# Optimization experiments

Hardware: AMD Instinct MI355X
Metric: run time of the kernel (lower is better)

The kernel has to match this reference:

```python
import jax, jax.numpy as jnp
import numpy as np

N, K = 50000, 16
D_IN, D_EDGE, D_HID, D_OUT = 128, 64, 32, 128


def setup_inputs() -> dict:
    key = jax.random.key(0)
    ks = jax.random.split(key, 10)
    s = lambda fan_in: 1.0 / np.sqrt(fan_in)
    return {
        'x': jax.random.normal(ks[0], (N, D_IN), jnp.float32),
        'neibs': jax.random.normal(ks[1], (N * K, D_IN), jnp.float32),
        'edge_emb': jax.random.normal(ks[2], (N * K, D_EDGE), jnp.float32),
        'mask': (jax.random.uniform(ks[3], (N, K)) < 0.3).astype(jnp.float32),
        # att: Linear(D_IN->H) -> tanh -> Linear(H->H); stored as [in,out]
        'W_att1_a': jax.random.uniform(ks[4], (D_IN, D_HID), jnp.float32, -s(D_IN), s(D_IN)),
        'W_att1_b': jax.random.uniform(ks[5], (D_HID, D_HID), jnp.float32, -s(D_HID), s(D_HID)),
        # att2 operates on concat(neibs, edge_emb)
        'W_att2_a': jax.random.uniform(ks[6], (D_IN + D_EDGE, D_HID), jnp.float32, -s(D_IN + D_EDGE), s(D_IN + D_EDGE)),
        'W_att2_b': jax.random.uniform(ks[7], (D_HID, D_HID), jnp.float32, -s(D_HID), s(D_HID)),
        'W_fc_x': jax.random.uniform(ks[8], (D_IN, D_OUT), jnp.float32, -s(D_IN), s(D_IN)),
        'W_fc_neib': jax.random.uniform(ks[9], (D_IN + D_EDGE, D_OUT), jnp.float32, -s(D_IN + D_EDGE), s(D_IN + D_EDGE)),
    }


def reference(x, neibs, edge_emb, mask, W_att1_a, W_att1_b, W_att2_a, W_att2_b, W_fc_x, W_fc_neib):
    n, k = mask.shape
    ne = jnp.concatenate([neibs, edge_emb], axis=1)            # [N*K, D_IN+D_EDGE]
    neib_att = jnp.tanh(ne @ W_att2_a) @ W_att2_b               # [N*K, H]
    x_att = jnp.tanh(x @ W_att1_a) @ W_att1_b                   # [N, H]
    ws = jnp.einsum('nkh,nh->nk', neib_att.reshape(n, k, -1), x_att)
    ws = jax.nn.softmax(ws + (-9999999.0) * mask, axis=1)       # masked softmax over neighbors
    agg_neib = jnp.einsum('nkd,nk->nd', ne.reshape(n, k, -1), ws)
    out = jnp.concatenate([x @ W_fc_x, agg_neib @ W_fc_neib], axis=1)  # concat_node=True
    return jax.nn.elu(out)  # dropout p=0.0 (eval), batchnorm=False
```

## Files before the change

### kernel.cpp

```cpp
#include <hip/hip_runtime.h>
#include <math.h>


typedef _Float16 half_t;
typedef __attribute__((ext_vector_type(4))) _Float16 half4_t;
typedef __attribute__((ext_vector_type(8))) _Float16 half8_t;
typedef __attribute__((ext_vector_type(4))) float f32x4;

#define NN   50000
#define GK   16
#define DIN  128
#define DED  64
#define DNE  192
#define G    8
#define NEP  200

#define WS_M    0
#define WS_W1A  4096
#define WS_W2A  12288
#define WS_WFX  24576
#define WS_WFN  57344

__device__ __forceinline__ void swz(const float* __restrict__ W, int ncol, int S,
                                    half_t* __restrict__ dst, int tid, int nth) {
  int T = ncol >> 4;
  int total = T * S * 512;
  for (int i = tid; i < total; i += nth) {
    int j = i & 7;
    int l = (i >> 3) & 63;
    int rest = i >> 9;
    int s = rest % S;
    int t = rest / S;
    int k = 32 * s + (l >> 4) * 8 + j;
    int n = 16 * t + (l & 15);
    dst[i] = (half_t)W[k * ncol + n];
  }
}

__global__ void setup_kernel(const float* __restrict__ W1a, const float* __restrict__ W1b,
                             const float* __restrict__ W2a, const float* __restrict__ W2b,
                             const float* __restrict__ Wfx, const float* __restrict__ Wfn,
                             unsigned char* __restrict__ ws) {
  int tid = blockIdx.x * blockDim.x + threadIdx.x;
  int nth = gridDim.x * blockDim.x;
  float* Mm = (float*)(ws + WS_M);
  for (int i = tid; i < 1024; i += nth) {
    int a = i >> 5, h = i & 31;
    float acc = 0.f;
    for (int h2 = 0; h2 < 32; ++h2)
      acc = fmaf(W1b[a * 32 + h2], W2b[h * 32 + h2], acc);
    Mm[i] = acc;
  }
  swz(W1a, 32, 4, (half_t*)(ws + WS_W1A), tid, nth);
  swz(W2a, 32, 6, (half_t*)(ws + WS_W2A), tid, nth);
  swz(Wfx, 128, 4, (half_t*)(ws + WS_WFX), tid, nth);
  swz(Wfn, 128, 6, (half_t*)(ws + WS_WFN), tid, nth);
}

__device__ __forceinline__ half8_t cvt8(float4 a, float4 b) {
  half8_t r;
  r[0] = (half_t)a.x; r[1] = (half_t)a.y; r[2] = (half_t)a.z; r[3] = (half_t)a.w;
  r[4] = (half_t)b.x; r[5] = (half_t)b.y; r[6] = (half_t)b.z; r[7] = (half_t)b.w;
  return r;
}

__device__ __forceinline__ float elu(float v) { return v > 0.f ? v : expm1f(v); }

__global__ __launch_bounds__(512, 4)
void attn_kernel(const float* __restrict__ x, const float* __restrict__ neibs,
                 const float* __restrict__ edge, const float* __restrict__ mask,
                 const unsigned char* __restrict__ ws, float* __restrict__ out) {
  __shared__ half_t neL[G * GK * NEP];
  __shared__ half_t aggL[16 * NEP];
  __shared__ float t1L[G][33];
  __shared__ float uL[G][33];
  __shared__ float scL[G][16];
  __shared__ float wsmL[G][16];

  const int tid = threadIdx.x;
  const int wave = tid >> 6;
  const int lane = tid & 63;
  const int l15 = lane & 15;
  const int q = lane >> 4;
  const int n0 = blockIdx.x * G;

  const float* Mm = (const float*)(ws + WS_M);
  const half_t* w1a = (const half_t*)(ws + WS_W1A);
  const half_t* w2a = (const half_t*)(ws + WS_W2A);
  const half_t* wfx = (const half_t*)(ws + WS_WFX);
  const half_t* wfn = (const half_t*)(ws + WS_WFN);

  {
    const float4* gn = (const float4*)(neibs + (size_t)n0 * (GK * DIN));
#pragma unroll
    for (int c = 0; c < 8; ++c) {
      int v = c * 512 + tid;
      float4 f = gn[v];
      int g = v >> 9, rem = v & 511, k = rem >> 5, d4 = rem & 31;
      half4_t h = { (half_t)f.x, (half_t)f.y, (half_t)f.z, (half_t)f.w };
      *(half4_t*)&neL[(g * GK + k) * NEP + d4 * 4] = h;
    }
    const float4* ge = (const float4*)(edge + (size_t)n0 * (GK * DED));
#pragma unroll
    for (int c = 0; c < 4; ++c) {
      int v = c * 512 + tid;
      float4 f = ge[v];
      int g = v >> 8, rem = v & 255, k = rem >> 4, d4 = rem & 15;
      half4_t h = { (half_t)f.x, (half_t)f.y, (half_t)f.z, (half_t)f.w };
      *(half4_t*)&neL[(g * GK + k) * NEP + DIN + d4 * 4] = h;
    }
    for (int i = tid; i < 16 * NEP / 2; i += 512)
      ((unsigned int*)aggL)[i] = 0u;
  }

  if (wave < 2) {
    f32x4 acc = {0.f, 0.f, 0.f, 0.f};
    int row = n0 + l15; if (row >= NN) row = NN - 1;
    const float* xrow = x + (size_t)row * DIN;
#pragma unroll
    for (int s = 0; s < 4; ++s) {
      float4 a0 = *(const float4*)(xrow + 32 * s + 8 * q);
      float4 a1 = *(const float4*)(xrow + 32 * s + 8 * q + 4);
      half8_t A = cvt8(a0, a1);
      half8_t B = *(const half8_t*)(w1a + ((size_t)(wave * 4 + s) * 64 + lane) * 8);
      acc = __builtin_amdgcn_mfma_f32_16x16x32_f16(A, B, acc, 0, 0, 0);
    }
#pragma unroll
    for (int r = 0; r < 4; ++r) {
      int g = 4 * q + r;
      if (g < G) t1L[g][wave * 16 + l15] = tanhf(acc[r]);
    }
  }
  __syncthreads();

  if (tid < G * 32) {
    int g = tid >> 5, h = tid & 31;
    float acc = 0.f;
#pragma unroll
    for (int a = 0; a < 32; ++a)
      acc = fmaf(t1L[g][a], Mm[a * 32 + h], acc);
    uL[g][h] = acc;
  }
  __syncthreads();

  {
    const int g = wave;
    f32x4 acc0 = {0.f, 0.f, 0.f, 0.f}, acc1 = {0.f, 0.f, 0.f, 0.f};
    const half_t* nerow = &neL[(g * GK + l15) * NEP];
#pragma unroll
    for (int s = 0; s < 6; ++s) {
      half8_t A  = *(const half8_t*)(nerow + 32 * s + 8 * q);
      half8_t B0 = *(const half8_t*)(w2a + ((size_t)(0 * 6 + s) * 64 + lane) * 8);
      half8_t B1 = *(const half8_t*)(w2a + ((size_t)(1 * 6 + s) * 64 + lane) * 8);
      acc0 = __builtin_amdgcn_mfma_f32_16x16x32_f16(A, B0, acc0, 0, 0, 0);
      acc1 = __builtin_amdgcn_mfma_f32_16x16x32_f16(A, B1, acc1, 0, 0, 0);
    }
    float u0 = uL[g][l15], u1 = uL[g][16 + l15];
    float sv[4];
#pragma unroll
    for (int r = 0; r < 4; ++r)
      sv[r] = tanhf(acc0[r]) * u0 + tanhf(acc1[r]) * u1;
#pragma unroll
    for (int off = 1; off <= 8; off <<= 1)
#pragma unroll
      for (int r = 0; r < 4; ++r)
        sv[r] += __shfl_xor(sv[r], off);
    if (l15 == 0)
#pragma unroll
      for (int r = 0; r < 4; ++r)
        scL[g][4 * q + r] = sv[r];
  }
  __syncthreads();

  {
    const int g = wave;
    float sc = -3.4e38f;
    if (lane < 16)
      sc = scL[g][lane] - 9999999.0f * mask[(size_t)(n0 + g) * GK + lane];
    float mx = sc;
#pragma unroll
    for (int off = 1; off <= 8; off <<= 1) mx = fmaxf(mx, __shfl_xor(mx, off));
    float e = (lane < 16) ? expf(sc - mx) : 0.f;
    float sm = e;
#pragma unroll
    for (int off = 1; off <= 8; off <<= 1) sm += __shfl_xor(sm, off);
    if (lane < 16) wsmL[g][lane] = e / sm;

    float a0 = 0.f, a1 = 0.f, a2 = 0.f;
    for (int k = 0; k < GK; ++k) {
      float wv = wsmL[g][k];
      const half_t* r_ = &neL[(g * GK + k) * NEP];
      a0 = fmaf(wv, (float)r_[lane], a0);
      a1 = fmaf(wv, (float)r_[64 + lane], a1);
      a2 = fmaf(wv, (float)r_[128 + lane], a2);
    }
    aggL[g * NEP + lane] = (half_t)a0;
    aggL[g * NEP + 64 + lane] = (half_t)a1;
    aggL[g * NEP + 128 + lane] = (half_t)a2;
  }
  __syncthreads();

  {
    f32x4 accx = {0.f, 0.f, 0.f, 0.f}, accn = {0.f, 0.f, 0.f, 0.f};
    int row = n0 + l15; if (row >= NN) row = NN - 1;
    const float* xrow = x + (size_t)row * DIN;
#pragma unroll
    for (int s = 0; s < 4; ++s) {
      float4 a0 = *(const float4*)(xrow + 32 * s + 8 * q);
      float4 a1 = *(const float4*)(xrow + 32 * s + 8 * q + 4);
      half8_t A = cvt8(a0, a1);
      half8_t B = *(const half8_t*)(wfx + ((size_t)(wave * 4 + s) * 64 + lane) * 8);
      accx = __builtin_amdgcn_mfma_f32_16x16x32_f16(A, B, accx, 0, 0, 0);
    }
#pragma unroll
    for (int s = 0; s < 6; ++s) {
      half8_t A = *(const half8_t*)(&aggL[l15 * NEP + 32 * s + 8 * q]);
      half8_t B = *(const half8_t*)(wfn + ((size_t)(wave * 6 + s) * 64 + lane) * 8);
      accn = __builtin_amdgcn_mfma_f32_16x16x32_f16(A, B, accn, 0, 0, 0);
    }
#pragma unroll
    for (int r = 0; r < 4; ++r) {
      int m = 4 * q + r;
      if (m < G) {
        size_t base = (size_t)(n0 + m) * 256;
        out[base + wave * 16 + l15] = elu(accx[r]);
        out[base + 128 + wave * 16 + l15] = elu(accn[r]);
      }
    }
  }
}

extern "C" void kernel_launch(void* const* d_in, const int* in_sizes, int n_in,
                              void* d_out, int out_size, void* d_ws, size_t ws_size,
                              hipStream_t stream) {
  const float* x     = (const float*)d_in[0];
  const float* neibs = (const float*)d_in[1];
  const float* edge  = (const float*)d_in[2];
  const float* mask  = (const float*)d_in[3];
  const float* W1a   = (const float*)d_in[4];
  const float* W1b   = (const float*)d_in[5];
  const float* W2a   = (const float*)d_in[6];
  const float* W2b   = (const float*)d_in[7];
  const float* Wfx   = (const float*)d_in[8];
  const float* Wfn   = (const float*)d_in[9];
  float* out = (float*)d_out;
  unsigned char* ws = (unsigned char*)d_ws;

  hipLaunchKernelGGL(setup_kernel, dim3(64), dim3(256), 0, stream,
                     W1a, W1b, W2a, W2b, Wfx, Wfn, ws);
  hipLaunchKernelGGL(attn_kernel, dim3(NN / G), dim3(512), 0, stream,
                     x, neibs, edge, mask, ws, out);
}
```

Measured before the change: 764.8 us.

## Split x-projection into pre-kernel and drop LDS staging of neighbor features

A new pre_kernel computes the x @ W_fc_x half of the output and the per-node attention query vector u. It stashes u temporarily in the not-yet-written second half of the output buffer. The attention kernel now assigns one node per wave and feeds neighbor and edge rows directly from global memory into the MFMA. It then re-reads them from global (expected to hit cache) for the softmax-weighted aggregation, instead of staging everything as fp16 in a large shared buffer. This cuts shared memory use sharply to raise occupancy, at the cost of a second pass over neighbor data and an extra kernel launch.

```diff
diff --git a/kernel.cpp b/kernel.cpp
--- a/kernel.cpp
+++ b/kernel.cpp
@@ -12,8 +12,6 @@
 #define DIN  128
 #define DED  64
 #define DNE  192
-#define G    8
-#define NEP  200
 
 #define WS_M    0
 #define WS_W1A  4096
@@ -66,167 +64,166 @@
 
 __device__ __forceinline__ float elu(float v) { return v > 0.f ? v : expm1f(v); }
 
-__global__ __launch_bounds__(512, 4)
-void attn_kernel(const float* __restrict__ x, const float* __restrict__ neibs,
-                 const float* __restrict__ edge, const float* __restrict__ mask,
-                 const unsigned char* __restrict__ ws, float* __restrict__ out) {
-  __shared__ half_t neL[G * GK * NEP];
-  __shared__ half_t aggL[16 * NEP];
-  __shared__ float t1L[G][33];
-  __shared__ float uL[G][33];
-  __shared__ float scL[G][16];
-  __shared__ float wsmL[G][16];
-
+__global__ __launch_bounds__(256, 4)
+void pre_kernel(const float* __restrict__ x, const unsigned char* __restrict__ ws,
+                float* __restrict__ out) {
+  __shared__ float t1L[64][33];
   const int tid = threadIdx.x;
-  const int wave = tid >> 6;
-  const int lane = tid & 63;
-  const int l15 = lane & 15;
-  const int q = lane >> 4;
-  const int n0 = blockIdx.x * G;
-
+  const int wave = tid >> 6, lane = tid & 63;
+  const int l15 = lane & 15, q = lane >> 4;
+  const int nb0 = blockIdx.x * 64;
+  const int n0 = nb0 + wave * 16;
   const float* Mm = (const float*)(ws + WS_M);
   const half_t* w1a = (const half_t*)(ws + WS_W1A);
-  const half_t* w2a = (const half_t*)(ws + WS_W2A);
   const half_t* wfx = (const half_t*)(ws + WS_WFX);
-  const half_t* wfn = (const half_t*)(ws + WS_WFN);
-
-  {
-    const float4* gn = (const float4*)(neibs + (size_t)n0 * (GK * DIN));
-#pragma unroll
-    for (int c = 0; c < 8; ++c) {
-      int v = c * 512 + tid;
-      float4 f = gn[v];
-      int g = v >> 9, rem = v & 511, k = rem >> 5, d4 = rem & 31;
-      half4_t h = { (half_t)f.x, (half_t)f.y, (half_t)f.z, (half_t)f.w };
-      *(half4_t*)&neL[(g * GK + k) * NEP + d4 * 4] = h;
-    }
-    const float4* ge = (const float4*)(edge + (size_t)n0 * (GK * DED));
-#pragma unroll
-    for (int c = 0; c < 4; ++c) {
-      int v = c * 512 + tid;
-      float4 f = ge[v];
-      int g = v >> 8, rem = v & 255, k = rem >> 4, d4 = rem & 15;
-      half4_t h = { (half_t)f.x, (half_t)f.y, (half_t)f.z, (half_t)f.w };
-      *(half4_t*)&neL[(g * GK + k) * NEP + DIN + d4 * 4] = h;
-    }
-    for (int i = tid; i < 16 * NEP / 2; i += 512)
-      ((unsigned int*)aggL)[i] = 0u;
-  }
-
-  if (wave < 2) {
-    f32x4 acc = {0.f, 0.f, 0.f, 0.f};
-    int row = n0 + l15; if (row >= NN) row = NN - 1;
-    const float* xrow = x + (size_t)row * DIN;
-#pragma unroll
-    for (int s = 0; s < 4; ++s) {
-      float4 a0 = *(const float4*)(xrow + 32 * s + 8 * q);
-      float4 a1 = *(const float4*)(xrow + 32 * s + 8 * q + 4);
-      half8_t A = cvt8(a0, a1);
-      half8_t B = *(const half8_t*)(w1a + ((size_t)(wave * 4 + s) * 64 + lane) * 8);
-      acc = __builtin_amdgcn_mfma_f32_16x16x32_f16(A, B, acc, 0, 0, 0);
-    }
-#pragma unroll
-    for (int r = 0; r < 4; ++r) {
-      int g = 4 * q + r;
-      if (g < G) t1L[g][wave * 16 + l15] = tanhf(acc[r]);
-    }
+
+  int row = n0 + l15; if (row >= NN) row = NN - 1;
+  const float* xrow = x + (size_t)row * DIN;
+  half8_t Ax[4];
+  f32x4 t0acc = {0.f, 0.f, 0.f, 0.f}, t1acc = {0.f, 0.f, 0.f, 0.f};
+#pragma unroll
+  for (int s = 0; s < 4; ++s) {
+    float4 a0 = *(const float4*)(xrow + 32 * s + 8 * q);
+    float4 a1 = *(const float4*)(xrow + 32 * s + 8 * q + 4);
+    Ax[s] = cvt8(a0, a1);
+    half8_t B0 = *(const half8_t*)(w1a + ((size_t)(0 * 4 + s) * 64 + lane) * 8);
+    half8_t B1 = *(const half8_t*)(w1a + ((size_t)(1 * 4 + s) * 64 + lane) * 8);
+    t0acc = __builtin_amdgcn_mfma_f32_16x16x32_f16(Ax[s], B0, t0acc, 0, 0, 0);
+    t1acc = __builtin_amdgcn_mfma_f32_16x16x32_f16(Ax[s], B1, t1acc, 0, 0, 0);
+  }
+#pragma unroll
+  for (int r = 0; r < 4; ++r) {
+    t1L[wave * 16 + 4 * q + r][l15]      = tanhf(t0acc[r]);
+    t1L[wave * 16 + 4 * q + r][16 + l15] = tanhf(t1acc[r]);
   }
   __syncthreads();
 
-  if (tid < G * 32) {
-    int g = tid >> 5, h = tid & 31;
+#pragma unroll
+  for (int i = 0; i < 8; ++i) {
+    int idx = i * 256 + tid;
+    int g = idx >> 5, h = idx & 31;
     float acc = 0.f;
 #pragma unroll
     for (int a = 0; a < 32; ++a)
       acc = fmaf(t1L[g][a], Mm[a * 32 + h], acc);
-    uL[g][h] = acc;
-  }
+    int n = nb0 + g;
+    if (n < NN) out[(size_t)n * 256 + 128 + h] = acc;
+  }
+
+#pragma unroll
+  for (int t = 0; t < 8; ++t) {
+    f32x4 acc = {0.f, 0.f, 0.f, 0.f};
+#pragma unroll
+    for (int s = 0; s < 4; ++s) {
+      half8_t B = *(const half8_t*)(wfx + ((size_t)(t * 4 + s) * 64 + lane) * 8);
+      acc = __builtin_amdgcn_mfma_f32_16x16x32_f16(Ax[s], B, acc, 0, 0, 0);
+    }
+#pragma unroll
+    for (int r = 0; r < 4; ++r) {
+      int m = n0 + 4 * q + r;
+      if (m < NN) out[(size_t)m * 256 + t * 16 + l15] = elu(acc[r]);
+    }
+  }
+}
+
+__global__ __launch_bounds__(512, 6)
+void attn_kernel(const float* __restrict__ neibs, const float* __restrict__ edge,
+                 const float* __restrict__ mask, const unsigned char* __restrict__ ws,
+                 float* __restrict__ out) {
+  __shared__ __align__(16) half_t aggL[16][200];
+  const int tid = threadIdx.x;
+  const int wave = tid >> 6, lane = tid & 63;
+  const int l15 = lane & 15, q = lane >> 4;
+  const int n = blockIdx.x * 8 + wave;
+  const half_t* w2a = (const half_t*)(ws + WS_W2A);
+  const half_t* wfn = (const half_t*)(ws + WS_WFN);
+
+  for (int i = tid; i < 800; i += 512)
+    ((unsigned int*)&aggL[8][0])[i] = 0u;
+
+  f32x4 acc0 = {0.f, 0.f, 0.f, 0.f}, acc1 = {0.f, 0.f, 0.f, 0.f};
+  const float* nbase = neibs + (size_t)n * (GK * DIN);
+  const float* ebase = edge + (size_t)n * (GK * DED);
+  const float* nrow = nbase + l15 * DIN;
+  const float* erow = ebase + l15 * DED;
+#pragma unroll
+  for (int s = 0; s < 4; ++s) {
+    float4 a0 = *(const float4*)(nrow + 32 * s + 8 * q);
+    float4 a1 = *(const float4*)(nrow + 32 * s + 8 * q + 4);
+    half8_t A = cvt8(a0, a1);
+    half8_t B0 = *(const half8_t*)(w2a + ((size_t)(0 * 6 + s) * 64 + lane) * 8);
+    half8_t B1 = *(const half8_t*)(w2a + ((size_t)(1 * 6 + s) * 64 + lane) * 8);
+    acc0 = __builtin_amdgcn_mfma_f32_16x16x32_f16(A, B0, acc0, 0, 0, 0);
+    acc1 = __builtin_amdgcn_mfma_f32_16x16x32_f16(A, B1, acc1, 0, 0, 0);
+  }
+#pragma unroll
+  for (int s = 0; s < 2; ++s) {
+    float4 a0 = *(const float4*)(erow + 32 * s + 8 * q);
+    float4 a1 = *(const float4*)(erow + 32 * s + 8 * q + 4);
+    half8_t A = cvt8(a0, a1);
+    half8_t B0 = *(const half8_t*)(w2a + ((size_t)(0 * 6 + 4 + s) * 64 + lane) * 8);
+    half8_t B1 = *(const half8_t*)(w2a + ((size_t)(1 * 6 + 4 + s) * 64 + lane) * 8);
+    acc0 = __builtin_amdgcn_mfma_f32_16x16x32_f16(A, B0, acc0, 0, 0, 0);
+    acc1 = __builtin_amdgcn_mfma_f32_16x16x32_f16(A, B1, acc1, 0, 0, 0);
+  }
+
+  const float u0 = out[(size_t)n * 256 + 128 + l15];
+  const float u1 = out[(size_t)n * 256 + 144 + l15];
+
+  float sv[4];
+#pragma unroll
+  for (int r = 0; r < 4; ++r)
+    sv[r] = tanhf(acc0[r]) * u0 + tanhf(acc1[r]) * u1;
+#pragma unroll
+  for (int off = 1; off <= 8; off <<= 1)
+#pragma unroll
+    for (int r = 0; r < 4; ++r)
+      sv[r] += __shfl_xor(sv[r], off);
+
+  float e[4];
+  float mx = -3.4e38f;
+#pragma unroll
+  for (int r = 0; r < 4; ++r) {
+    sv[r] -= 9999999.0f * mask[(size_t)n * GK + 4 * q + r];
+    mx = fmaxf(mx, sv[r]);
+  }
+  mx = fmaxf(mx, __shfl_xor(mx, 16));
+  mx = fmaxf(mx, __shfl_xor(mx, 32));
+  float sm = 0.f;
+#pragma unroll
+  for (int r = 0; r < 4; ++r) { e[r] = expf(sv[r] - mx); sm += e[r]; }
+  sm += __shfl_xor(sm, 16);
+  sm += __shfl_xor(sm, 32);
+  const float rs = 1.0f / sm;
+#pragma unroll
+  for (int r = 0; r < 4; ++r) e[r] *= rs;
+
+  float a0 = 0.f, a1 = 0.f, a2 = 0.f;
+#pragma unroll
+  for (int k = 0; k < GK; ++k) {
+    float wv = __shfl(e[k & 3], (k & 12) << 2);
+    a0 = fmaf(wv, nbase[k * DIN + lane], a0);
+    a1 = fmaf(wv, nbase[k * DIN + 64 + lane], a1);
+    a2 = fmaf(wv, ebase[k * DED + lane], a2);
+  }
+  aggL[wave][lane] = (half_t)a0;
+  aggL[wave][64 + lane] = (half_t)a1;
+  aggL[wave][128 + lane] = (half_t)a2;
   __syncthreads();
 
-  {
-    const int g = wave;
-    f32x4 acc0 = {0.f, 0.f, 0.f, 0.f}, acc1 = {0.f, 0.f, 0.f, 0.f};
-    const half_t* nerow = &neL[(g * GK + l15) * NEP];
-#pragma unroll
-    for (int s = 0; s < 6; ++s) {
-      half8_t A  = *(const half8_t*)(nerow + 32 * s + 8 * q);
-      half8_t B0 = *(const half8_t*)(w2a + ((size_t)(0 * 6 + s) * 64 + lane) * 8);
-      half8_t B1 = *(const half8_t*)(w2a + ((size_t)(1 * 6 + s) * 64 + lane) * 8);
-      acc0 = __builtin_amdgcn_mfma_f32_16x16x32_f16(A, B0, acc0, 0, 0, 0);
-      acc1 = __builtin_amdgcn_mfma_f32_16x16x32_f16(A, B1, acc1, 0, 0, 0);
-    }
-    float u0 = uL[g][l15], u1 = uL[g][16 + l15];
-    float sv[4];
-#pragma unroll
-    for (int r = 0; r < 4; ++r)
-      sv[r] = tanhf(acc0[r]) * u0 + tanhf(acc1[r]) * u1;
-#pragma unroll
-    for (int off = 1; off <= 8; off <<= 1)
-#pragma unroll
-      for (int r = 0; r < 4; ++r)
-        sv[r] += __shfl_xor(sv[r], off);
-    if (l15 == 0)
-#pragma unroll
-      for (int r = 0; r < 4; ++r)
-        scL[g][4 * q + r] = sv[r];
-  }
-  __syncthreads();
-
-  {
-    const int g = wave;
-    float sc = -3.4e38f;
-    if (lane < 16)
-      sc = scL[g][lane] - 9999999.0f * mask[(size_t)(n0 + g) * GK + lane];
-    float mx = sc;
-#pragma unroll
-    for (int off = 1; off <= 8; off <<= 1) mx = fmaxf(mx, __shfl_xor(mx, off));
-    float e = (lane < 16) ? expf(sc - mx) : 0.f;
-    float sm = e;
-#pragma unroll
-    for (int off = 1; off <= 8; off <<= 1) sm += __shfl_xor(sm, off);
-    if (lane < 16) wsmL[g][lane] = e / sm;
-
-    float a0 = 0.f, a1 = 0.f, a2 = 0.f;
-    for (int k = 0; k < GK; ++k) {
-      float wv = wsmL[g][k];
-      const half_t* r_ = &neL[(g * GK + k) * NEP];
-      a0 = fmaf(wv, (float)r_[lane], a0);
-      a1 = fmaf(wv, (float)r_[64 + lane], a1);
-      a2 = fmaf(wv, (float)r_[128 + lane], a2);
-    }
-    aggL[g * NEP + lane] = (half_t)a0;
-    aggL[g * NEP + 64 + lane] = (half_t)a1;
-    aggL[g * NEP + 128 + lane] = (half_t)a2;
-  }
-  __syncthreads();
-
-  {
-    f32x4 accx = {0.f, 0.f, 0.f, 0.f}, accn = {0.f, 0.f, 0.f, 0.f};
-    int row = n0 + l15; if (row >= NN) row = NN - 1;
-    const float* xrow = x + (size_t)row * DIN;
-#pragma unroll
-    for (int s = 0; s < 4; ++s) {
-      float4 a0 = *(const float4*)(xrow + 32 * s + 8 * q);
-      float4 a1 = *(const float4*)(xrow + 32 * s + 8 * q + 4);
-      half8_t A = cvt8(a0, a1);
-      half8_t B = *(const half8_t*)(wfx + ((size_t)(wave * 4 + s) * 64 + lane) * 8);
-      accx = __builtin_amdgcn_mfma_f32_16x16x32_f16(A, B, accx, 0, 0, 0);
-    }
-#pragma unroll
-    for (int s = 0; s < 6; ++s) {
-      half8_t A = *(const half8_t*)(&aggL[l15 * NEP + 32 * s + 8 * q]);
-      half8_t B = *(const half8_t*)(wfn + ((size_t)(wave * 6 + s) * 64 + lane) * 8);
-      accn = __builtin_amdgcn_mfma_f32_16x16x32_f16(A, B, accn, 0, 0, 0);
-    }
-#pragma unroll
-    for (int r = 0; r < 4; ++r) {
-      int m = 4 * q + r;
-      if (m < G) {
-        size_t base = (size_t)(n0 + m) * 256;
-        out[base + wave * 16 + l15] = elu(accx[r]);
-        out[base + 128 + wave * 16 + l15] = elu(accn[r]);
-      }
-    }
+  f32x4 accn = {0.f, 0.f, 0.f, 0.f};
+#pragma unroll
+  for (int s = 0; s < 6; ++s) {
+    half8_t A = *(const half8_t*)(&aggL[l15][32 * s + 8 * q]);
+    half8_t B = *(const half8_t*)(wfn + ((size_t)(wave * 6 + s) * 64 + lane) * 8);
+    accn = __builtin_amdgcn_mfma_f32_16x16x32_f16(A, B, accn, 0, 0, 0);
+  }
+  const size_t ob = (size_t)blockIdx.x * 8 * 256;
+#pragma unroll
+  for (int r = 0; r < 4; ++r) {
+    int m = 4 * q + r;
+    if (m < 8)
+      out[ob + (size_t)m * 256 + 128 + wave * 16 + l15] = elu(accn[r]);
   }
 }
 
@@ -248,6 +245,8 @@
 
   hipLaunchKernelGGL(setup_kernel, dim3(64), dim3(256), 0, stream,
                      W1a, W1b, W2a, W2b, Wfx, Wfn, ws);
-  hipLaunchKernelGGL(attn_kernel, dim3(NN / G), dim3(512), 0, stream,
-                     x, neibs, edge, mask, ws, out);
-}
+  hipLaunchKernelGGL(pre_kernel, dim3((NN + 63) / 64), dim3(256), 0, stream,
+                     x, ws, out);
+  hipLaunchKernelGGL(attn_kernel, dim3(NN / 8), dim3(512), 0, stream,
+                     neibs, edge, mask, ws, out);
+}
```

Result: faster. 738.7 us (-3.4%).
